# Performance work log

Measured on AMD Instinct MI355X. Metric: run time of the kernel, lower is better.

## Reference

```python
import jax, jax.numpy as jnp
import numpy as np

B, C, T, H, NCLS = 512, 22, 1000, 64, 4


def setup_inputs() -> dict:
    key = jax.random.key(0)
    ks = jax.random.split(key, 8)
    s_ih = 1.0 / np.sqrt(H)
    x = jax.random.normal(ks[0], (B, C, T), dtype=jnp.float32)
    # PyTorch LSTM params: gate order [i, f, g, o], each of size H
    W_ih = jax.random.uniform(ks[1], (4 * H, C), minval=-s_ih, maxval=s_ih, dtype=jnp.float32)
    W_hh = jax.random.uniform(ks[2], (4 * H, H), minval=-s_ih, maxval=s_ih, dtype=jnp.float32)
    b_ih = jax.random.uniform(ks[3], (4 * H,), minval=-s_ih, maxval=s_ih, dtype=jnp.float32)
    b_hh = jax.random.uniform(ks[4], (4 * H,), minval=-s_ih, maxval=s_ih, dtype=jnp.float32)
    s_fc = 1.0 / np.sqrt(H * T)
    W_fc = jax.random.uniform(ks[5], (NCLS, H * T), minval=-s_fc, maxval=s_fc, dtype=jnp.float32)
    b_fc = jax.random.uniform(ks[6], (NCLS,), minval=-s_fc, maxval=s_fc, dtype=jnp.float32)
    return {"x": x, "W_ih": W_ih, "W_hh": W_hh, "b_ih": b_ih, "b_hh": b_hh,
            "W_fc": W_fc, "b_fc": b_fc}


def _lstm(xs, W_ih, W_hh, b_ih, b_hh):
    # xs: [B, T, C] -> outputs [B, T, H]
    b = xs.shape[0]
    # precompute input projections for all timesteps: [T, B, 4H]
    x_proj = jnp.einsum('btc,gc->tbg', xs, W_ih) + (b_ih + b_hh)
    h0 = jnp.zeros((b, W_hh.shape[1]), xs.dtype)
    c0 = jnp.zeros_like(h0)

    def step(carry, xp):
        h, c = carry
        gates = xp + h @ W_hh.T  # [B, 4H]
        i, f, g, o = jnp.split(gates, 4, axis=-1)
        i = jax.nn.sigmoid(i)
        f = jax.nn.sigmoid(f)
        g = jnp.tanh(g)
        o = jax.nn.sigmoid(o)
        c = f * c + i * g
        h = o * jnp.tanh(c)
        return (h, c), h

    _, hs = jax.lax.scan(step, (h0, c0), x_proj)  # hs: [T, B, H]
    return jnp.transpose(hs, (1, 0, 2))  # [B, T, H]


def reference(x, W_ih, W_hh, b_ih, b_hh, W_fc, b_fc):
    xs = jnp.transpose(x, (0, 2, 1))  # [B, T, C]  (permute(0,2,1))
    hs = _lstm(xs, W_ih, W_hh, b_ih, b_hh)  # [B, T, H]
    flat = hs.reshape(hs.shape[0], -1)  # [B, T*H], time-major per row
    logits = flat @ W_fc.T + b_fc  # [B, 4]
    return jax.nn.softmax(logits, axis=1)
```

## Files before the change

kernel.cpp:

```cpp
#include <hip/hip_runtime.h>

#define BB   512
#define CC   22
#define TT   1000
#define HH   64
#define NCLS 4
#define FCW  (TT * HH)
#define TBX  200
#define TCF  250

typedef _Float16 f16;
typedef __attribute__((ext_vector_type(2))) _Float16 h2;

__device__ __forceinline__ float sigm(float x) {
    float e = __expf(-x);
    return __builtin_amdgcn_rcpf(1.0f + e);
}
__device__ __forceinline__ float tanh_(float x) {
    float e = __expf(-2.0f * fabsf(x));
    float r = (1.0f - e) * __builtin_amdgcn_rcpf(1.0f + e);
    return copysignf(r, x);
}
__device__ __forceinline__ h2 u2h(unsigned u) {
    union { unsigned u; h2 h; } c; c.u = u; return c.h;
}
__device__ __forceinline__ unsigned h2u(h2 h) {
    union { unsigned u; h2 h; } c; c.h = h; return c.u;
}
__device__ __forceinline__ unsigned pack2(float a, float b) {
    union { unsigned u; h2 h; } c;
    c.h = h2{(f16)a, (f16)b};
    return c.u;
}

__global__ __launch_bounds__(256) void xproj(
    const float* __restrict__ x,
    const float* __restrict__ W_ih,
    const float* __restrict__ b_ih,
    const float* __restrict__ b_hh,
    uint2* __restrict__ xp)
{
    __shared__ __align__(16) h2 xt[TBX][12];

    const int tid = threadIdx.x;
    const int t0  = blockIdx.x * TBX;
    const int b   = blockIdx.y;
    const int hid = tid & 63;
    const int tsub = tid >> 6;

    if (tid < TBX) {
        const float* gx = x + (size_t)b * (CC * TT) + t0 + tid;
        union { h2 h[12]; uint4 q[3]; } U;
        #pragma unroll
        for (int k = 0; k < 11; ++k)
            U.h[k] = h2{(f16)gx[(2 * k) * TT], (f16)gx[(2 * k + 1) * TT]};
        U.h[11] = h2{(f16)0.0f, (f16)0.0f};
        uint4* dst = (uint4*)&xt[tid][0];
        dst[0] = U.q[0]; dst[1] = U.q[1]; dst[2] = U.q[2];
    }

    unsigned wih[4][11];
    float bias[4];
    #pragma unroll
    for (int g = 0; g < 4; ++g) {
        const float* wi = W_ih + (g * HH + hid) * CC;
        #pragma unroll
        for (int k = 0; k < 11; ++k)
            wih[g][k] = h2u(h2{(f16)wi[2 * k], (f16)wi[2 * k + 1]});
        bias[g] = b_ih[g * HH + hid] + b_hh[g * HH + hid];
    }
    __syncthreads();

    uint2* op = xp + ((size_t)b * TT + t0) * 64 + hid;
    for (int t = tsub; t < TBX; t += 4) {
        union { uint4 q[3]; h2 h[12]; } X;
        const uint4* xr = (const uint4*)&xt[t][0];
        X.q[0] = xr[0]; X.q[1] = xr[1]; X.q[2] = xr[2];
        float a0 = bias[0], a1 = bias[1], a2 = bias[2], a3 = bias[3];
        #pragma unroll
        for (int k = 0; k < 11; ++k) {
            a0 = __builtin_amdgcn_fdot2(X.h[k], u2h(wih[0][k]), a0, false);
            a1 = __builtin_amdgcn_fdot2(X.h[k], u2h(wih[1][k]), a1, false);
            a2 = __builtin_amdgcn_fdot2(X.h[k], u2h(wih[2][k]), a2, false);
            a3 = __builtin_amdgcn_fdot2(X.h[k], u2h(wih[3][k]), a3, false);
        }
        op[(size_t)t * 64] = uint2{pack2(a0, a1), pack2(a2, a3)};
    }
}

__global__ __attribute__((amdgpu_waves_per_eu(1, 1)))
__launch_bounds__(64) void lstm_rec(
    const uint2* __restrict__ xp,
    const float* __restrict__ W_hh,
    const float* __restrict__ W_fc,
    const float* __restrict__ b_fc,
    float* __restrict__ out)
{
    __shared__ __align__(16) f16 hst[TCF][HH];

    const int lane = threadIdx.x;
    const int r    = blockIdx.x;

    unsigned whh[4][32];
    #pragma unroll
    for (int g = 0; g < 4; ++g) {
        const float* wr = W_hh + (g * HH + lane) * HH;
        #pragma unroll
        for (int k = 0; k < 32; ++k)
            whh[g][k] = h2u(h2{(f16)wr[2 * k], (f16)wr[2 * k + 1]});
    }
    #pragma unroll
    for (int g = 0; g < 4; ++g)
        #pragma unroll
        for (int k = 0; k < 32; ++k) asm volatile("" : "+v"(whh[g][k]));

    hst[TCF - 1][lane] = (f16)0.0f;
    float c = 0.0f;
    float fc0 = 0.f, fc1 = 0.f, fc2 = 0.f, fc3 = 0.f;
    const uint2* px = xp + (size_t)r * TT * HH + lane;

    uint2 xvA = px[0];
    uint2 xvB = px[HH];
    uint2 xvC = px[2 * HH];

    for (int chunk = 0; chunk < 4; ++chunk) {
        const int T0 = chunk * TCF;

        for (int tt = 0; tt < TCF; ++tt) {
            const int t = T0 + tt;

            const int tp = (t + 3 < TT) ? t + 3 : TT - 1;
            const uint2 xvN = px[(size_t)tp * HH];

            const int pr = (tt == 0) ? TCF - 1 : tt - 1;
            union { uint4 q[8]; h2 h[32]; } H;
            const uint4* hr = (const uint4*)&hst[pr][0];
            #pragma unroll
            for (int i = 0; i < 8; ++i) H.q[i] = hr[i];

            const h2 pif = u2h(xvA.x), pgo = u2h(xvA.y);
            float a0 = (float)pif[0], a1 = (float)pif[1];
            float a2 = (float)pgo[0], a3 = (float)pgo[1];
            #pragma unroll
            for (int k = 0; k < 32; ++k) {
                a0 = __builtin_amdgcn_fdot2(H.h[k], u2h(whh[0][k]), a0, false);
                a1 = __builtin_amdgcn_fdot2(H.h[k], u2h(whh[1][k]), a1, false);
                a2 = __builtin_amdgcn_fdot2(H.h[k], u2h(whh[2][k]), a2, false);
                a3 = __builtin_amdgcn_fdot2(H.h[k], u2h(whh[3][k]), a3, false);
            }

            const float iv = sigm(a0), fv = sigm(a1);
            const float gv = tanh_(a2), ov = sigm(a3);
            c = fv * c + iv * gv;
            const float h = ov * tanh_(c);

            hst[tt][lane] = (f16)h;

            xvA = xvB; xvB = xvC; xvC = xvN;
        }

        const float* w0 = W_fc + 0 * FCW + (size_t)T0 * HH + lane;
        const float* w1 = W_fc + 1 * FCW + (size_t)T0 * HH + lane;
        const float* w2 = W_fc + 2 * FCW + (size_t)T0 * HH + lane;
        const float* w3 = W_fc + 3 * FCW + (size_t)T0 * HH + lane;
        for (int tt = 0; tt < TCF; ++tt) {
            const float hv = (float)hst[tt][lane];
            fc0 += hv * w0[(size_t)tt * HH];
            fc1 += hv * w1[(size_t)tt * HH];
            fc2 += hv * w2[(size_t)tt * HH];
            fc3 += hv * w3[(size_t)tt * HH];
        }
    }

    #pragma unroll
    for (int off = 32; off; off >>= 1) {
        fc0 += __shfl_down(fc0, off);
        fc1 += __shfl_down(fc1, off);
        fc2 += __shfl_down(fc2, off);
        fc3 += __shfl_down(fc3, off);
    }
    if (lane == 0) {
        const float l0 = fc0 + b_fc[0], l1 = fc1 + b_fc[1];
        const float l2 = fc2 + b_fc[2], l3 = fc3 + b_fc[3];
        const float m  = fmaxf(fmaxf(l0, l1), fmaxf(l2, l3));
        const float e0 = __expf(l0 - m), e1 = __expf(l1 - m);
        const float e2 = __expf(l2 - m), e3 = __expf(l3 - m);
        const float is = __builtin_amdgcn_rcpf(e0 + e1 + e2 + e3);
        float4 o; o.x = e0 * is; o.y = e1 * is; o.z = e2 * is; o.w = e3 * is;
        *(float4*)(out + r * NCLS) = o;
    }
}

#define TC   250
#define NCHUNK (TT / TC)
#define XROW 12

__global__ __attribute__((amdgpu_waves_per_eu(1, 1)))
__launch_bounds__(64) void lstm_fb(
    const float* __restrict__ x, const float* __restrict__ W_ih,
    const float* __restrict__ W_hh, const float* __restrict__ b_ih,
    const float* __restrict__ b_hh, const float* __restrict__ W_fc,
    const float* __restrict__ b_fc, float* __restrict__ out)
{
    __shared__ __align__(16) h2  xs[TC][XROW];
    __shared__ __align__(16) f16 hbuf[HH];

    const int lane = threadIdx.x;
    const int r    = blockIdx.x;

    unsigned whh[4][32];
    unsigned wih[4][11];
    float bias[4];
    #pragma unroll
    for (int g = 0; g < 4; ++g) {
        const int row = g * HH + lane;
        const float* wr = W_hh + row * HH;
        #pragma unroll
        for (int k = 0; k < 32; ++k)
            whh[g][k] = h2u(h2{(f16)wr[2 * k], (f16)wr[2 * k + 1]});
        const float* wi = W_ih + row * CC;
        #pragma unroll
        for (int k = 0; k < 11; ++k)
            wih[g][k] = h2u(h2{(f16)wi[2 * k], (f16)wi[2 * k + 1]});
        bias[g] = b_ih[row] + b_hh[row];
    }
    #pragma unroll
    for (int g = 0; g < 4; ++g) {
        #pragma unroll
        for (int k = 0; k < 32; ++k) asm volatile("" : "+v"(whh[g][k]));
        #pragma unroll
        for (int k = 0; k < 11; ++k) asm volatile("" : "+v"(wih[g][k]));
        asm volatile("" : "+v"(bias[g]));
    }

    hbuf[lane] = (f16)0.0f;
    float c = 0.0f;
    float fc0 = 0.f, fc1 = 0.f, fc2 = 0.f, fc3 = 0.f;
    const float* p0 = W_fc + 0 * FCW + lane;
    const float* p1 = W_fc + 1 * FCW + lane;
    const float* p2 = W_fc + 2 * FCW + lane;
    const float* p3 = W_fc + 3 * FCW + lane;
    const float* xrow = x + (size_t)r * (CC * TT);

    for (int chunk = 0; chunk < NCHUNK; ++chunk) {
        for (int tb = 0; tb < TC; tb += 64) {
            const int t = tb + lane;
            if (t < TC) {
                const float* gx = xrow + chunk * TC + t;
                union { h2 h[XROW]; uint4 q[3]; } U;
                #pragma unroll
                for (int k = 0; k < 11; ++k)
                    U.h[k] = h2{(f16)gx[(2 * k) * TT], (f16)gx[(2 * k + 1) * TT]};
                U.h[11] = h2{(f16)0.0f, (f16)0.0f};
                uint4* dst = (uint4*)&xs[t][0];
                dst[0] = U.q[0]; dst[1] = U.q[1]; dst[2] = U.q[2];
            }
        }
        for (int tt = 0; tt < TC; ++tt) {
            union { uint4 q[8]; h2 h[32]; } H;
            const uint4* hr = (const uint4*)hbuf;
            #pragma unroll
            for (int i = 0; i < 8; ++i) H.q[i] = hr[i];
            union { uint4 q[3]; h2 h[XROW]; } X;
            const uint4* xr = (const uint4*)&xs[tt][0];
            X.q[0] = xr[0]; X.q[1] = xr[1]; X.q[2] = xr[2];
            float w0 = *p0, w1 = *p1, w2 = *p2, w3 = *p3;
            p0 += HH; p1 += HH; p2 += HH; p3 += HH;
            float a0 = bias[0], a1 = bias[1], a2 = bias[2], a3 = bias[3];
            #pragma unroll
            for (int k = 0; k < 11; ++k) {
                a0 = __builtin_amdgcn_fdot2(X.h[k], u2h(wih[0][k]), a0, false);
                a1 = __builtin_amdgcn_fdot2(X.h[k], u2h(wih[1][k]), a1, false);
                a2 = __builtin_amdgcn_fdot2(X.h[k], u2h(wih[2][k]), a2, false);
                a3 = __builtin_amdgcn_fdot2(X.h[k], u2h(wih[3][k]), a3, false);
            }
            #pragma unroll
            for (int k = 0; k < 32; ++k) {
                a0 = __builtin_amdgcn_fdot2(H.h[k], u2h(whh[0][k]), a0, false);
                a1 = __builtin_amdgcn_fdot2(H.h[k], u2h(whh[1][k]), a1, false);
                a2 = __builtin_amdgcn_fdot2(H.h[k], u2h(whh[2][k]), a2, false);
                a3 = __builtin_amdgcn_fdot2(H.h[k], u2h(whh[3][k]), a3, false);
            }
            const float iv = sigm(a0), fv = sigm(a1);
            const float gv = tanh_(a2), ov = sigm(a3);
            c = fv * c + iv * gv;
            const float h = ov * tanh_(c);
            fc0 += h * w0; fc1 += h * w1; fc2 += h * w2; fc3 += h * w3;
            hbuf[lane] = (f16)h;
        }
    }
    #pragma unroll
    for (int off = 32; off; off >>= 1) {
        fc0 += __shfl_down(fc0, off);
        fc1 += __shfl_down(fc1, off);
        fc2 += __shfl_down(fc2, off);
        fc3 += __shfl_down(fc3, off);
    }
    if (lane == 0) {
        const float l0 = fc0 + b_fc[0], l1 = fc1 + b_fc[1];
        const float l2 = fc2 + b_fc[2], l3 = fc3 + b_fc[3];
        const float m  = fmaxf(fmaxf(l0, l1), fmaxf(l2, l3));
        const float e0 = __expf(l0 - m), e1 = __expf(l1 - m);
        const float e2 = __expf(l2 - m), e3 = __expf(l3 - m);
        const float is = __builtin_amdgcn_rcpf(e0 + e1 + e2 + e3);
        float4 o; o.x = e0 * is; o.y = e1 * is; o.z = e2 * is; o.w = e3 * is;
        *(float4*)(out + r * NCLS) = o;
    }
}

extern "C" void kernel_launch(void* const* d_in, const int* in_sizes, int n_in,
                              void* d_out, int out_size, void* d_ws, size_t ws_size,
                              hipStream_t stream) {
    const float* x    = (const float*)d_in[0];
    const float* W_ih = (const float*)d_in[1];
    const float* W_hh = (const float*)d_in[2];
    const float* b_ih = (const float*)d_in[3];
    const float* b_hh = (const float*)d_in[4];
    const float* W_fc = (const float*)d_in[5];
    const float* b_fc = (const float*)d_in[6];
    float* out = (float*)d_out;

    const size_t need = (size_t)BB * TT * HH * 4 * sizeof(f16);
    if (d_ws != nullptr && ws_size >= need) {
        uint2* xp = (uint2*)d_ws;
        xproj<<<dim3(TT / TBX, BB), 256, 0, stream>>>(x, W_ih, b_ih, b_hh, xp);
        lstm_rec<<<BB, 64, 0, stream>>>(xp, W_hh, W_fc, b_fc, out);
    } else {
        lstm_fb<<<BB, 64, 0, stream>>>(x, W_ih, W_hh, b_ih, b_hh, W_fc, b_fc, out);
    }
}
```

Baseline: 655.4 us.

## Broadcast hidden state via DPP/swizzle cross-lane ops instead of LDS round-trip

Replaces the per-step LDS read of the full previous hidden vector with an in-register butterfly broadcast built from DPP, ds_swizzle and a shuffle. W_hh columns are permuted per lane with an XOR slot mask so each lane's permuted h pairs line up with its weights. The aim is to remove LDS load latency from the serial recurrence's critical path, at the cost of many cross-lane moves per step. The xproj time tile size is also halved.

New measurement: 732.3 us. 11.7% more time.

```diff
diff --git a/kernel.cpp b/kernel.cpp
--- a/kernel.cpp
+++ b/kernel.cpp
@@ -6,7 +6,7 @@
 #define HH   64
 #define NCLS 4
 #define FCW  (TT * HH)
-#define TBX  200
+#define TBX  100
 #define TCF  250
 
 typedef _Float16 f16;
@@ -31,6 +31,13 @@
     union { unsigned u; h2 h; } c;
     c.h = h2{(f16)a, (f16)b};
     return c.u;
+}
+
+#define DPP(v, ctrl) __builtin_amdgcn_mov_dpp((v), (ctrl), 0xF, 0xF, false)
+
+__device__ __forceinline__ int slotmask(int r) {
+    return ((r & 1) ? 2 : 0) ^ ((r & 2) ? 7 : 0) ^ ((r & 4) ? 15 : 0)
+         ^ ((r & 8) ? 16 : 0) ^ ((r & 16) ? 32 : 0);
 }
 
 __global__ __launch_bounds__(256) void xproj(
@@ -106,15 +113,18 @@
     for (int g = 0; g < 4; ++g) {
         const float* wr = W_hh + (g * HH + lane) * HH;
         #pragma unroll
-        for (int k = 0; k < 32; ++k)
-            whh[g][k] = h2u(h2{(f16)wr[2 * k], (f16)wr[2 * k + 1]});
+        for (int k = 0; k < 32; ++k) {
+            const int m    = slotmask(k);
+            const int hid0 = lane ^ m;
+            const int hid1 = hid0 ^ 1;
+            whh[g][k] = pack2(wr[hid0], wr[hid1]);
+        }
     }
     #pragma unroll
     for (int g = 0; g < 4; ++g)
         #pragma unroll
         for (int k = 0; k < 32; ++k) asm volatile("" : "+v"(whh[g][k]));
 
-    hst[TCF - 1][lane] = (f16)0.0f;
     float c = 0.0f;
     float fc0 = 0.f, fc1 = 0.f, fc2 = 0.f, fc3 = 0.f;
     const uint2* px = xp + (size_t)r * TT * HH + lane;
@@ -123,6 +133,10 @@
     uint2 xvB = px[HH];
     uint2 xvC = px[2 * HH];
 
+    unsigned Wr[32];
+    #pragma unroll
+    for (int k = 0; k < 32; ++k) Wr[k] = 0u;
+
     for (int chunk = 0; chunk < 4; ++chunk) {
         const int T0 = chunk * TCF;
 
@@ -131,22 +145,16 @@
 
             const int tp = (t + 3 < TT) ? t + 3 : TT - 1;
             const uint2 xvN = px[(size_t)tp * HH];
-
-            const int pr = (tt == 0) ? TCF - 1 : tt - 1;
-            union { uint4 q[8]; h2 h[32]; } H;
-            const uint4* hr = (const uint4*)&hst[pr][0];
-            #pragma unroll
-            for (int i = 0; i < 8; ++i) H.q[i] = hr[i];
 
             const h2 pif = u2h(xvA.x), pgo = u2h(xvA.y);
             float a0 = (float)pif[0], a1 = (float)pif[1];
             float a2 = (float)pgo[0], a3 = (float)pgo[1];
             #pragma unroll
             for (int k = 0; k < 32; ++k) {
-                a0 = __builtin_amdgcn_fdot2(H.h[k], u2h(whh[0][k]), a0, false);
-                a1 = __builtin_amdgcn_fdot2(H.h[k], u2h(whh[1][k]), a1, false);
-                a2 = __builtin_amdgcn_fdot2(H.h[k], u2h(whh[2][k]), a2, false);
-                a3 = __builtin_amdgcn_fdot2(H.h[k], u2h(whh[3][k]), a3, false);
+                a0 = __builtin_amdgcn_fdot2(u2h(Wr[k]), u2h(whh[0][k]), a0, false);
+                a1 = __builtin_amdgcn_fdot2(u2h(Wr[k]), u2h(whh[1][k]), a1, false);
+                a2 = __builtin_amdgcn_fdot2(u2h(Wr[k]), u2h(whh[2][k]), a2, false);
+                a3 = __builtin_amdgcn_fdot2(u2h(Wr[k]), u2h(whh[3][k]), a3, false);
             }
 
             const float iv = sigm(a0), fv = sigm(a1);
@@ -155,6 +163,22 @@
             const float h = ov * tanh_(c);
 
             hst[tt][lane] = (f16)h;
+
+            const int hp_ = DPP(__float_as_int(h), 0xB1);
+            const unsigned P = pack2(h, __int_as_float(hp_));
+            Wr[0]  = P;
+            Wr[16] = (unsigned)__shfl_xor((int)P, 32);
+            Wr[8]  = (unsigned)__builtin_amdgcn_ds_swizzle((int)Wr[0],  0x401F);
+            Wr[24] = (unsigned)__builtin_amdgcn_ds_swizzle((int)Wr[16], 0x401F);
+            #pragma unroll
+            for (int i = 0; i < 32; i += 8)
+                Wr[i + 4] = (unsigned)DPP((int)Wr[i], 0x140);
+            #pragma unroll
+            for (int i = 0; i < 32; i += 4)
+                Wr[i + 2] = (unsigned)DPP((int)Wr[i], 0x141);
+            #pragma unroll
+            for (int i = 0; i < 32; i += 2)
+                Wr[i + 1] = (unsigned)DPP((int)Wr[i], 0x4E);
 
             xvA = xvB; xvB = xvC; xvC = xvN;
         }
```
